# Performance work log

Measured on AMD Instinct MI355X. Metric: run time of the kernel, lower is better.

Reference implementation:

```python
import jax, jax.numpy as jnp
import numpy as np

N, D = 16384, 128
NUM_CLASSES = 100


def setup_inputs() -> dict:
    key = jax.random.key(0)
    k1, k2 = jax.random.split(key)
    feature_bank = jax.random.normal(k1, (N, D), dtype=jnp.float32)
    label_bank = jax.random.randint(k2, (N,), 0, NUM_CLASSES, dtype=jnp.int64)
    return {"feature_bank": feature_bank, "label_bank": label_bank}


def reference(feature_bank, label_bank):
    n = feature_bank.shape[0]
    sq = jnp.sum(feature_bank * feature_bank, axis=1, keepdims=True)  # [N, 1]
    distmat = sq + sq.T - 2.0 * (feature_bank @ feature_bank.T)
    # mask self-matches: set diagonal to the global max of distmat
    dmax = jnp.max(distmat)
    idx = jnp.arange(n)
    distmat = distmat.at[idx, idx].set(dmax)
    # nearest neighbor per row
    predicted = jnp.argmin(distmat, axis=1)  # [N]
    # recall@1: fraction of instances whose NN shares the label
    matches = (label_bank[predicted] == label_bank)
    recall_k = jnp.sum(matches).astype(jnp.float32) / n
    return recall_k
```

## Files before the change

kernel.cpp:

```cpp
#include <hip/hip_runtime.h>


typedef __bf16 bf16x8 __attribute__((ext_vector_type(8)));
typedef float f32x4 __attribute__((ext_vector_type(4)));

#define NN 16384
#define MFMA16(A, B, C) __builtin_amdgcn_mfma_f32_16x16x32_bf16(A, B, C, 0, 0, 0)
#define GLDS(gsrc, ldst)                                                              \
  __builtin_amdgcn_global_load_lds((const __attribute__((address_space(1))) void*)(gsrc), \
                                   (__attribute__((address_space(3))) void*)(ldst), 16, 0, 0)

__global__ __launch_bounds__(256) void sq_kernel(const float* __restrict__ feat,
                                                 float* __restrict__ sq) {
  int gid = blockIdx.x * 256 + threadIdx.x;
  int row = gid >> 6;
  int lane = threadIdx.x & 63;
  float2 v = reinterpret_cast<const float2*>(feat + (size_t)row * 128)[lane];
  float s = v.x * v.x + v.y * v.y;
#pragma unroll
  for (int off = 32; off > 0; off >>= 1) s += __shfl_xor(s, off, 64);
  if (lane == 0) sq[row] = s;
}

__global__ __launch_bounds__(256) void convert_kernel(const float* __restrict__ feat,
                                                      bf16x8* __restrict__ Ph,
                                                      bf16x8* __restrict__ Pl) {
  int chunk = blockIdx.x * 256 + threadIdx.x;
  int l = chunk & 63;
  int ks = (chunk >> 6) & 3;
  int g = chunk >> 8;
  int row = g * 16 + (l & 15);
  int k0 = ks * 32 + (l >> 4) * 8;
  const float4* s = reinterpret_cast<const float4*>(feat + (size_t)row * 128 + k0);
  float4 v0 = s[0], v1 = s[1];
  float xs[8] = {v0.x, v0.y, v0.z, v0.w, v1.x, v1.y, v1.z, v1.w};
  bf16x8 hv, lv;
#pragma unroll
  for (int e = 0; e < 8; ++e) {
    float x = xs[e];
    __bf16 h = (__bf16)x;
    hv[e] = h;
    lv[e] = (__bf16)(x - (float)h);
  }
  Ph[chunk] = hv;
  Pl[chunk] = lv;
}

__global__ __launch_bounds__(512, 4) void nn_mfma(const bf16x8* __restrict__ Ph,
                                                  const bf16x8* __restrict__ Pl,
                                                  const float* __restrict__ sq,
                                                  float* __restrict__ bestD,
                                                  int* __restrict__ bestI) {
  __shared__ bf16x8 BhL[2][1024];
  const int bid = blockIdx.x;
  const int slice = bid & 7;
  const int panel = bid >> 3;
  const int tid = threadIdx.x;
  const int w = tid >> 6;
  const int lane = tid & 63;
  const int lq = lane >> 4;
  const int lc = lane & 15;

  bf16x8 Ah0[4], Al0[4], Ah1[4], Al1[4];
  {
    int gA = panel * 16 + w * 2;
#pragma unroll
    for (int ks = 0; ks < 4; ++ks) {
      Ah0[ks] = Ph[(gA * 4 + ks) * 64 + lane];
      Al0[ks] = Pl[(gA * 4 + ks) * 64 + lane];
      Ah1[ks] = Ph[((gA + 1) * 4 + ks) * 64 + lane];
      Al1[ks] = Pl[((gA + 1) * 4 + ks) * 64 + lane];
    }
  }

  auto stage = [&](int nbuf, int tt) {
    const int cgi = w >> 1;
    const int gcol = slice * 128 + tt * 4 + cgi;
    const int ks0 = (w & 1) * 2;
    bf16x8* dst = &BhL[nbuf][cgi * 256];
#pragma unroll
    for (int ks = ks0; ks < ks0 + 2; ++ks) {
      size_t srcoff = ((size_t)((gcol * 4 + ks) * 64 + lane)) * 16;
      GLDS((const char*)Ph + srcoff, dst + ks * 64);
    }
  };

  float best0[4], best1[4];
  int bidx0[4], bidx1[4];
#pragma unroll
  for (int r = 0; r < 4; ++r) {
    best0[r] = 3.4e38f; best1[r] = 3.4e38f;
    bidx0[r] = 0; bidx1[r] = 0;
  }

  stage(0, 0);
  __syncthreads();

  int buf = 0;
  const int ig0 = panel * 256 + w * 32 + lq * 4;

  for (int t = 0; t < 32; ++t) {
    const int jb = slice * 2048 + t * 64;
    float sqc[4];
#pragma unroll
    for (int cg = 0; cg < 4; ++cg) sqc[cg] = sq[jb + cg * 16 + lc];
    if (t < 31) stage(buf ^ 1, t + 1);

#pragma unroll
    for (int cg = 0; cg < 4; ++cg) {
      f32x4 a0 = {}, a1 = {};
#pragma unroll
      for (int ks = 0; ks < 4; ++ks) {
        bf16x8 bh = BhL[buf][cg * 256 + ks * 64 + lane];
        a0 = MFMA16(Ah0[ks], bh, a0);
        a1 = MFMA16(Ah1[ks], bh, a1);
        a0 = MFMA16(Al0[ks], bh, a0);
        a1 = MFMA16(Al1[ks], bh, a1);
      }
      const int j = jb + cg * 16 + lc;
#pragma unroll
      for (int r = 0; r < 4; ++r) {
        float d0 = fmaf(-2.0f, a0[r], sqc[cg]);
        if (j != ig0 + r && d0 < best0[r]) { best0[r] = d0; bidx0[r] = j; }
        float d1 = fmaf(-2.0f, a1[r], sqc[cg]);
        if (j != ig0 + 16 + r && d1 < best1[r]) { best1[r] = d1; bidx1[r] = j; }
      }
    }

    __syncthreads();
    buf ^= 1;
  }

#pragma unroll
  for (int r = 0; r < 4; ++r) {
    float d0 = best0[r], d1 = best1[r];
    int i0 = bidx0[r], i1 = bidx1[r];
#pragma unroll
    for (int off = 1; off < 16; off <<= 1) {
      float od = __shfl_xor(d0, off); int oi = __shfl_xor(i0, off);
      if (od < d0 || (od == d0 && oi < i0)) { d0 = od; i0 = oi; }
      od = __shfl_xor(d1, off); oi = __shfl_xor(i1, off);
      if (od < d1 || (od == d1 && oi < i1)) { d1 = od; i1 = oi; }
    }
    if (lc == 0) {
      bestD[slice * NN + ig0 + r] = d0;
      bestI[slice * NN + ig0 + r] = i0;
      bestD[slice * NN + ig0 + 16 + r] = d1;
      bestI[slice * NN + ig0 + 16 + r] = i1;
    }
  }
}

__global__ __launch_bounds__(256) void combine_kernel(const float* __restrict__ bestD,
                                                      const int* __restrict__ bestI,
                                                      const int* __restrict__ labels,
                                                      int* __restrict__ count) {
  int r = blockIdx.x * 256 + threadIdx.x;
  float d = bestD[r];
  int i = bestI[r];
#pragma unroll
  for (int s = 1; s < 8; ++s) {
    float ds = bestD[s * NN + r];
    int is = bestI[s * NN + r];
    if (ds < d || (ds == d && is < i)) { d = ds; i = is; }
  }
  bool match = (labels[i] == labels[r]);
  unsigned long long mb = __ballot(match);
  if ((threadIdx.x & 63) == 0) atomicAdd(count, (int)__popcll(mb));
}

__global__ void finalize_kernel(const int* __restrict__ count, float* __restrict__ out) {
  out[0] = (float)(*count) * (1.0f / 16384.0f);
}

extern "C" void kernel_launch(void* const* d_in, const int* in_sizes, int n_in,
                              void* d_out, int out_size, void* d_ws, size_t ws_size,
                              hipStream_t stream) {
  const float* feat = (const float*)d_in[0];
  const int* labels = (const int*)d_in[1];
  float* out = (float*)d_out;
  char* ws = (char*)d_ws;

  int* count = (int*)ws;
  float* sq = (float*)(ws + 1024);
  float* bestD = (float*)(ws + (1 << 19));
  int* bestI = (int*)(ws + (1 << 20));
  bf16x8* Ph = (bf16x8*)(ws + (2 << 20));
  bf16x8* Pl = (bf16x8*)(ws + (6 << 20));

  hipMemsetAsync(count, 0, sizeof(int), stream);
  sq_kernel<<<NN / 4, 256, 0, stream>>>(feat, sq);
  convert_kernel<<<1024, 256, 0, stream>>>(feat, Ph, Pl);
  nn_mfma<<<512, 512, 0, stream>>>(Ph, Pl, sq, bestD, bestI);
  combine_kernel<<<NN / 256, 256, 0, stream>>>(bestD, bestI, labels, count);
  finalize_kernel<<<1, 1, 0, stream>>>(count, out);
}
```

Before: 133.4 us.

## Exploit distance symmetry with upper-triangle tiles and packed atomicMin reductions

The all-pairs kernel now launches only the upper-triangular 256x256 tile pairs (2080 blocks) instead of the full grid. Each off-diagonal tile updates both its row minima and its column minima. Results are merged through 64-bit atomicMin on keys that pack the float distance bits with the index, which removes the per-slice bestD/bestI buffers and the 8-way combine. A +256 offset on the squared norms keeps distances positive so their float bits order correctly as unsigned integers. This roughly halves the MFMA work but adds many global 64-bit atomics per tile plus an extra cross-lane shuffle. The column-direction distance is also not exactly symmetric with the row-direction one, because only the row side of the product uses the hi/lo split.

Measured after the change: 134.1 us. No clear change (+0.6%).

```diff
diff --git a/kernel.cpp b/kernel.cpp
--- a/kernel.cpp
+++ b/kernel.cpp
@@ -19,7 +19,7 @@
   float s = v.x * v.x + v.y * v.y;
 #pragma unroll
   for (int off = 32; off > 0; off >>= 1) s += __shfl_xor(s, off, 64);
-  if (lane == 0) sq[row] = s;
+  if (lane == 0) sq[row] = s + 256.0f;
 }
 
 __global__ __launch_bounds__(256) void convert_kernel(const float* __restrict__ feat,
@@ -46,15 +46,14 @@
   Pl[chunk] = lv;
 }
 
-__global__ __launch_bounds__(512, 4) void nn_mfma(const bf16x8* __restrict__ Ph,
-                                                  const bf16x8* __restrict__ Pl,
-                                                  const float* __restrict__ sq,
-                                                  float* __restrict__ bestD,
-                                                  int* __restrict__ bestI) {
+__global__ __launch_bounds__(512, 4) void nn_tri(const bf16x8* __restrict__ Ph,
+                                                 const bf16x8* __restrict__ Pl,
+                                                 const float* __restrict__ sq,
+                                                 unsigned long long* __restrict__ rowKey) {
   __shared__ bf16x8 BhL[2][1024];
-  const int bid = blockIdx.x;
-  const int slice = bid & 7;
-  const int panel = bid >> 3;
+  int b = blockIdx.x, P = 0;
+  while (b >= 64 - P) { b -= 64 - P; ++P; }
+  const int Q = P + b;
   const int tid = threadIdx.x;
   const int w = tid >> 6;
   const int lane = tid & 63;
@@ -63,7 +62,7 @@
 
   bf16x8 Ah0[4], Al0[4], Ah1[4], Al1[4];
   {
-    int gA = panel * 16 + w * 2;
+    int gA = P * 16 + w * 2;
 #pragma unroll
     for (int ks = 0; ks < 4; ++ks) {
       Ah0[ks] = Ph[(gA * 4 + ks) * 64 + lane];
@@ -73,9 +72,17 @@
     }
   }
 
+  const int ig0 = P * 256 + w * 32 + lq * 4;
+  float sqA0[4], sqA1[4];
+#pragma unroll
+  for (int r = 0; r < 4; ++r) {
+    sqA0[r] = sq[ig0 + r];
+    sqA1[r] = sq[ig0 + 16 + r];
+  }
+
   auto stage = [&](int nbuf, int tt) {
     const int cgi = w >> 1;
-    const int gcol = slice * 128 + tt * 4 + cgi;
+    const int gcol = Q * 16 + tt * 4 + cgi;
     const int ks0 = (w & 1) * 2;
     bf16x8* dst = &BhL[nbuf][cgi * 256];
 #pragma unroll
@@ -97,14 +104,14 @@
   __syncthreads();
 
   int buf = 0;
-  const int ig0 = panel * 256 + w * 32 + lq * 4;
-
-  for (int t = 0; t < 32; ++t) {
-    const int jb = slice * 2048 + t * 64;
+  const int diagT = (P == Q) ? (w >> 1) : -1;
+
+  for (int t = 0; t < 4; ++t) {
+    const int jb = Q * 256 + t * 64;
     float sqc[4];
 #pragma unroll
     for (int cg = 0; cg < 4; ++cg) sqc[cg] = sq[jb + cg * 16 + lc];
-    if (t < 31) stage(buf ^ 1, t + 1);
+    if (t < 3) stage(buf ^ 1, t + 1);
 
 #pragma unroll
     for (int cg = 0; cg < 4; ++cg) {
@@ -118,12 +125,48 @@
         a1 = MFMA16(Al1[ks], bh, a1);
       }
       const int j = jb + cg * 16 + lc;
-#pragma unroll
-      for (int r = 0; r < 4; ++r) {
-        float d0 = fmaf(-2.0f, a0[r], sqc[cg]);
-        if (j != ig0 + r && d0 < best0[r]) { best0[r] = d0; bidx0[r] = j; }
-        float d1 = fmaf(-2.0f, a1[r], sqc[cg]);
-        if (j != ig0 + 16 + r && d1 < best1[r]) { best1[r] = d1; bidx1[r] = j; }
+      if (t != diagT) {
+#pragma unroll
+        for (int r = 0; r < 4; ++r) {
+          float d0 = fmaf(-2.0f, a0[r], sqc[cg]);
+          if (d0 < best0[r]) { best0[r] = d0; bidx0[r] = j; }
+          float d1 = fmaf(-2.0f, a1[r], sqc[cg]);
+          if (d1 < best1[r]) { best1[r] = d1; bidx1[r] = j; }
+        }
+      } else {
+#pragma unroll
+        for (int r = 0; r < 4; ++r) {
+          float d0 = fmaf(-2.0f, a0[r], sqc[cg]);
+          if (j != ig0 + r && d0 < best0[r]) { best0[r] = d0; bidx0[r] = j; }
+          float d1 = fmaf(-2.0f, a1[r], sqc[cg]);
+          if (j != ig0 + 16 + r && d1 < best1[r]) { best1[r] = d1; bidx1[r] = j; }
+        }
+      }
+      if (P != Q) {
+        float m = fmaf(-2.0f, a0[0], sqA0[0]);
+        int mi = ig0;
+#pragma unroll
+        for (int r = 1; r < 4; ++r) {
+          float d = fmaf(-2.0f, a0[r], sqA0[r]);
+          if (d < m) { m = d; mi = ig0 + r; }
+        }
+#pragma unroll
+        for (int r = 0; r < 4; ++r) {
+          float d = fmaf(-2.0f, a1[r], sqA1[r]);
+          if (d < m) { m = d; mi = ig0 + 16 + r; }
+        }
+#pragma unroll
+        for (int off = 16; off <= 32; off <<= 1) {
+          float od = __shfl_xor(m, off);
+          int oi = __shfl_xor(mi, off);
+          if (od < m || (od == m && oi < mi)) { m = od; mi = oi; }
+        }
+        if (lq == 0) {
+          unsigned long long key =
+              ((unsigned long long)__builtin_bit_cast(unsigned int, m) << 14) |
+              (unsigned long long)mi;
+          atomicMin(&rowKey[j], key);
+        }
       }
     }
 
@@ -143,27 +186,23 @@
       if (od < d1 || (od == d1 && oi < i1)) { d1 = od; i1 = oi; }
     }
     if (lc == 0) {
-      bestD[slice * NN + ig0 + r] = d0;
-      bestI[slice * NN + ig0 + r] = i0;
-      bestD[slice * NN + ig0 + 16 + r] = d1;
-      bestI[slice * NN + ig0 + 16 + r] = i1;
-    }
-  }
-}
-
-__global__ __launch_bounds__(256) void combine_kernel(const float* __restrict__ bestD,
-                                                      const int* __restrict__ bestI,
+      unsigned long long k0 =
+          ((unsigned long long)__builtin_bit_cast(unsigned int, d0) << 14) |
+          (unsigned long long)i0;
+      atomicMin(&rowKey[ig0 + r], k0);
+      unsigned long long k1 =
+          ((unsigned long long)__builtin_bit_cast(unsigned int, d1) << 14) |
+          (unsigned long long)i1;
+      atomicMin(&rowKey[ig0 + 16 + r], k1);
+    }
+  }
+}
+
+__global__ __launch_bounds__(256) void combine_kernel(const unsigned long long* __restrict__ rowKey,
                                                       const int* __restrict__ labels,
                                                       int* __restrict__ count) {
   int r = blockIdx.x * 256 + threadIdx.x;
-  float d = bestD[r];
-  int i = bestI[r];
-#pragma unroll
-  for (int s = 1; s < 8; ++s) {
-    float ds = bestD[s * NN + r];
-    int is = bestI[s * NN + r];
-    if (ds < d || (ds == d && is < i)) { d = ds; i = is; }
-  }
+  int i = (int)(rowKey[r] & 0x3FFFull);
   bool match = (labels[i] == labels[r]);
   unsigned long long mb = __ballot(match);
   if ((threadIdx.x & 63) == 0) atomicAdd(count, (int)__popcll(mb));
@@ -183,15 +222,15 @@
 
   int* count = (int*)ws;
   float* sq = (float*)(ws + 1024);
-  float* bestD = (float*)(ws + (1 << 19));
-  int* bestI = (int*)(ws + (1 << 20));
+  unsigned long long* rowKey = (unsigned long long*)(ws + (1 << 19));
   bf16x8* Ph = (bf16x8*)(ws + (2 << 20));
   bf16x8* Pl = (bf16x8*)(ws + (6 << 20));
 
   hipMemsetAsync(count, 0, sizeof(int), stream);
+  hipMemsetAsync(rowKey, 0xFF, NN * sizeof(unsigned long long), stream);
   sq_kernel<<<NN / 4, 256, 0, stream>>>(feat, sq);
   convert_kernel<<<1024, 256, 0, stream>>>(feat, Ph, Pl);
-  nn_mfma<<<512, 512, 0, stream>>>(Ph, Pl, sq, bestD, bestI);
-  combine_kernel<<<NN / 256, 256, 0, stream>>>(bestD, bestI, labels, count);
+  nn_tri<<<2080, 512, 0, stream>>>(Ph, Pl, sq, rowKey);
+  combine_kernel<<<NN / 256, 256, 0, stream>>>(rowKey, labels, count);
   finalize_kernel<<<1, 1, 0, stream>>>(count, out);
 }
```
